# Optimization experiments

Measured on AMD Instinct MI355X. Metric: run time of the kernel, lower is better.

## Reference

```python
import jax, jax.numpy as jnp
import numpy as np

N, E, IN_DIM, HID, HEADS, OUT_DIM, T = 50000, 200000, 32, 64, 4, 32, 3
NEG_SLOPE = 0.2  # PyG GATv2Conv default


def setup_inputs() -> dict:
    key = jax.random.key(0)
    ks = jax.random.split(key, 16)
    s = 0.1
    return {
        "feat": jax.random.normal(ks[0], (N, IN_DIM), jnp.float32),
        "W_in": jax.random.normal(ks[1], (IN_DIM, HID), jnp.float32) * s,
        "b_in": jnp.zeros((HID,), jnp.float32),
        "Wl": jax.random.normal(ks[2], (2 * HID, HEADS * HID), jnp.float32) * s,
        "bl": jnp.zeros((HEADS * HID,), jnp.float32),
        "Wr": jax.random.normal(ks[3], (2 * HID, HEADS * HID), jnp.float32) * s,
        "br": jnp.zeros((HEADS * HID,), jnp.float32),
        "att": jax.random.normal(ks[4], (HEADS, HID), jnp.float32) * s,
        "b_conv": jnp.zeros((HEADS * HID,), jnp.float32),
        "Wg": jax.random.normal(ks[5], (HID, OUT_DIM), jnp.float32) * s,
        "bg": jnp.zeros((OUT_DIM,), jnp.float32),
        "edge_index": jax.random.randint(ks[6], (2, E), 0, N, jnp.int32),
        "node_mask": jax.random.randint(ks[7], (N,), 0, T + 1, jnp.int32),
        "current_state": jax.random.randint(ks[8], (N,), 0, 2, jnp.int32),
    }


def reference(feat, W_in, b_in, Wl, bl, Wr, br, att, b_conv, Wg, bg,
              edge_index, node_mask, current_state):
    # add self loops (GATv2Conv add_self_loops=True)
    loops = jnp.arange(N, dtype=edge_index.dtype)
    src = jnp.concatenate([edge_index[0], loops])  # [E+N]
    dst = jnp.concatenate([edge_index[1], loops])

    h0 = feat @ W_in + b_in  # [N, HID]
    bias_sum = b_conv.reshape(HEADS, HID).sum(0)  # heads are summed after bias add

    def step(h, i):
        active = node_mask > i  # [N] bool: nodes updated at this step
        x = jnp.concatenate([h, h0], axis=-1)  # [N, 2*HID]
        xl = (x @ Wl + bl).reshape(N, HEADS, HID)  # source transform
        xr = (x @ Wr + br).reshape(N, HEADS, HID)  # target transform
        e_act = active[src] & active[dst]  # edge alive iff both endpoints active
        s = jax.nn.leaky_relu(xl[src] + xr[dst], NEG_SLOPE)  # [E+N, H, C]
        score = jnp.einsum('ehc,hc->eh', s, att)  # [E+N, H]
        score = jnp.where(e_act[:, None], score, -1e30)
        smax = jax.lax.stop_gradient(
            jax.ops.segment_max(score, dst, num_segments=N))  # [N, H]
        ex = jnp.exp(score - smax[dst]) * e_act[:, None].astype(score.dtype)
        denom = jax.ops.segment_sum(ex, dst, num_segments=N)  # [N, H]
        alpha = ex / jnp.maximum(denom[dst], 1e-16)  # segment softmax per dst
        msg = alpha[:, :, None] * xl[src]  # [E+N, H, C]
        agg = jax.ops.segment_sum(msg, dst, num_segments=N)  # [N, H, C]
        out = jnp.tanh(agg.sum(1) + bias_sum)  # sum over heads, then Tanh
        return jnp.where(active[:, None], out, h), None

    h, _ = jax.lax.scan(step, h0, jnp.arange(T))
    # original returns g_embed(h[current_state]); fixed-shape variant: mask rows
    out = (h @ Wg + bg) * (current_state[:, None] > 0).astype(h.dtype)
    return out
```

## Files before the change

kernel.cpp:

```cpp
#include <hip/hip_runtime.h>
#include <hip/hip_bf16.h>

#define NN      50000
#define EE      200000
#define IN_DIM  32
#define HID     64
#define HEADS   4
#define OUTD    32
#define TSTEPS  3

typedef unsigned short bf16_t;
typedef __attribute__((ext_vector_type(8))) short  short8;
typedef __attribute__((ext_vector_type(4))) float  floatx4;

__device__ __forceinline__ float b2f(bf16_t u) {
    union { unsigned int i; float f; } v; v.i = ((unsigned int)u) << 16; return v.f;
}
__device__ __forceinline__ bf16_t f2b(float f) {
    union { float f; unsigned int i; } v; v.f = f;
    unsigned int r = v.i + 0x7FFF + ((v.i >> 16) & 1);
    return (bf16_t)(r >> 16);
}

__global__ void k_probe(const void* __restrict__ W_in, int* __restrict__ flag,
                        int* __restrict__ mbuf) {
    __shared__ int bad;
    int t = threadIdx.x;
    if (t == 0) bad = 0;
    if (t < 16) mbuf[t] = 0;
    __syncthreads();
    const bf16_t* p = (const bf16_t*)W_in;
    int mybad = 0;
    for (int i = t; i < IN_DIM * HID; i += 256) {
        float v = b2f(p[i]);
        if (v != v || fabsf(v) > 100.f) mybad = 1;
    }
    if (mybad) atomicOr(&bad, 1);
    __syncthreads();
    if (t == 0) *flag = bad ? 0 : 1;
}

__global__ __launch_bounds__(256) void k_cvt_small(
        const void* W_in, const void* b_in, const void* att, const void* bconv,
        const void* Wg, const void* bg,
        float* Winf, float* binf, float* attf, float* bcf, float* Wgf, float* bgf,
        const int* __restrict__ flag) {
    int i = blockIdx.x * 256 + threadIdx.x;
    int f = *flag;
    const void* src; float* dst; int off;
    if      (i < 2048) { src = W_in;  dst = Winf; off = i; }
    else if (i < 2112) { src = b_in;  dst = binf; off = i - 2048; }
    else if (i < 2368) { src = att;   dst = attf; off = i - 2112; }
    else if (i < 2624) { src = bconv; dst = bcf;  off = i - 2368; }
    else if (i < 4672) { src = Wg;    dst = Wgf;  off = i - 2624; }
    else if (i < 4704) { src = bg;    dst = bgf;  off = i - 4672; }
    else return;
    dst[off] = f ? b2f(((const bf16_t*)src)[off]) : ((const float*)src)[off];
}

__global__ __launch_bounds__(256) void k_wt(const void* Wl_raw, const void* Wr_raw,
                                            const void* bl_raw, const void* br_raw,
                                            bf16_t* __restrict__ Wt,
                                            float* __restrict__ bb,
                                            const int* __restrict__ flag) {
    int i = blockIdx.x * 256 + threadIdx.x;
    if (i >= 512 * 128) return;
    int f = *flag;
    int n = i >> 7, k = i & 127;
    const void* W = (n < 256) ? Wl_raw : Wr_raw;
    int nn = (n < 256) ? n : n - 256;
    float v = f ? b2f(((const bf16_t*)W)[k * 256 + nn])
                : ((const float*)W)[k * 256 + nn];
    Wt[i] = f2b(v);
    if (k == 0) {
        const void* b = (n < 256) ? bl_raw : br_raw;
        bb[n] = f ? b2f(((const bf16_t*)b)[nn]) : ((const float*)b)[nn];
    }
}

__global__ __launch_bounds__(256) void k_zero(int* __restrict__ p, int n) {
    int i = blockIdx.x * 256 + threadIdx.x;
    if (i < n) p[i] = 0;
}

__global__ __launch_bounds__(256) void k_hist(const int* __restrict__ dst,
                                              int* __restrict__ deg, int n) {
    int i = blockIdx.x * 256 + threadIdx.x;
    if (i < n) atomicAdd(&deg[dst[i]], 1);
}

__global__ __launch_bounds__(256) void k_scan_partial(const int* __restrict__ deg,
                                                      int* __restrict__ part, int n) {
    __shared__ int sd[256];
    int t = threadIdx.x;
    int base = blockIdx.x * 1024;
    int s = 0;
#pragma unroll
    for (int j = 0; j < 4; j++) {
        int i = base + t * 4 + j;
        if (i < n) s += deg[i];
    }
    sd[t] = s; __syncthreads();
    for (int off = 128; off > 0; off >>= 1) {
        if (t < off) sd[t] += sd[t + off];
        __syncthreads();
    }
    if (t == 0) part[blockIdx.x] = sd[0];
}

__global__ void k_scan_chunks(int* part, int nch) {
    if (threadIdx.x == 0 && blockIdx.x == 0) {
        int acc = 0;
        for (int i = 0; i < nch; i++) { int v = part[i]; part[i] = acc; acc += v; }
        part[nch] = acc;
    }
}

__global__ __launch_bounds__(256) void k_scan_final(const int* __restrict__ deg,
                                                    const int* __restrict__ part,
                                                    int* __restrict__ row_ptr,
                                                    int* __restrict__ cursor,
                                                    int n, int nch) {
    __shared__ int sc[256];
    int t = threadIdx.x;
    int base = blockIdx.x * 1024;
    int v[4]; int s = 0;
#pragma unroll
    for (int j = 0; j < 4; j++) {
        int i = base + t * 4 + j;
        v[j] = (i < n) ? deg[i] : 0;
        s += v[j];
    }
    sc[t] = s; __syncthreads();
    for (int off = 1; off < 256; off <<= 1) {
        int add = (t >= off) ? sc[t - off] : 0;
        __syncthreads();
        sc[t] += add;
        __syncthreads();
    }
    int run = sc[t] - s + part[blockIdx.x];
#pragma unroll
    for (int j = 0; j < 4; j++) {
        int i = base + t * 4 + j;
        if (i < n) { row_ptr[i] = run; cursor[i] = run; run += v[j]; }
    }
    if (blockIdx.x == 0 && t == 0) row_ptr[n] = part[nch];
}

__global__ __launch_bounds__(256) void k_scatter(const int* __restrict__ src,
                                                 const int* __restrict__ dst,
                                                 int* __restrict__ cursor,
                                                 int* __restrict__ col, int n) {
    int i = blockIdx.x * 256 + threadIdx.x;
    if (i < n) {
        int d = dst[i];
        int pos = atomicAdd(&cursor[d], 1);
        col[pos] = src[i];
    }
}

__global__ __launch_bounds__(256) void k_mhist(const int* __restrict__ mask,
                                               int* __restrict__ mbuf) {
    __shared__ int wcnt[4][4];
    int t = threadIdx.x, wid = t >> 6, lane = t & 63;
    int i = blockIdx.x * 256 + t;
    bool valid = i < NN;
    int v = 0;
    if (valid) { int m = mask[i]; v = m < 0 ? 0 : (m > 3 ? 3 : m); }
#pragma unroll
    for (int b = 0; b < 4; b++) {
        unsigned long long mm = __ballot(valid && v == b);
        if (lane == 0) wcnt[wid][b] = __popcll(mm);
    }
    __syncthreads();
    if (t < 4) {
        int s = wcnt[0][t] + wcnt[1][t] + wcnt[2][t] + wcnt[3][t];
        if (s) atomicAdd(&mbuf[t], s);
    }
}

__global__ void k_moff(int* mbuf) {
    if (threadIdx.x == 0 && blockIdx.x == 0) {
        int c1 = mbuf[1], c2 = mbuf[2], c3 = mbuf[3];
        mbuf[7] = 0;
        mbuf[6] = c3;
        mbuf[5] = c3 + c2;
        mbuf[4] = c3 + c2 + c1;
        mbuf[8] = c3 + c2 + c1;
        mbuf[9] = c3 + c2;
        mbuf[10] = c3;
    }
}

__global__ __launch_bounds__(256) void k_mscatter(const int* __restrict__ mask,
                                                  int* __restrict__ mbuf,
                                                  int* __restrict__ order) {
    __shared__ int wcnt[4][4];
    __shared__ int bbase[4];
    int t = threadIdx.x, wid = t >> 6, lane = t & 63;
    int i = blockIdx.x * 256 + t;
    bool valid = i < NN;
    int v = 0;
    if (valid) { int m = mask[i]; v = m < 0 ? 0 : (m > 3 ? 3 : m); }
    int rank = 0;
#pragma unroll
    for (int b = 0; b < 4; b++) {
        unsigned long long mm = __ballot(valid && v == b);
        if (valid && v == b)
            rank = __popcll(mm & ((lane == 0) ? 0ull : (~0ull >> (64 - lane))));
        if (lane == 0) wcnt[wid][b] = __popcll(mm);
    }
    __syncthreads();
    if (t < 4) {
        int tot = wcnt[0][t] + wcnt[1][t] + wcnt[2][t] + wcnt[3][t];
        bbase[t] = atomicAdd(&mbuf[4 + t], tot);
    }
    __syncthreads();
    if (valid) {
        int wpre = 0;
        for (int ww = 0; ww < wid; ww++) wpre += wcnt[ww][v];
        order[bbase[v] + wpre + rank] = i;
    }
}

__global__ __launch_bounds__(256) void k_h0(const void* __restrict__ feat_raw,
                                            const float* __restrict__ W_in,
                                            const float* __restrict__ b_in,
                                            float* __restrict__ h0,
                                            float* __restrict__ h,
                                            const int* __restrict__ flag) {
    __shared__ float Ws[IN_DIM * HID];
    __shared__ float bs[HID];
    int t = threadIdx.x;
    for (int i = t; i < IN_DIM * HID; i += 256) Ws[i] = W_in[i];
    if (t < HID) bs[t] = b_in[t];
    __syncthreads();
    int node = blockIdx.x * 4 + (t >> 6);
    int c = t & 63;
    if (node >= NN) return;
    int f = *flag;
    float acc = bs[c];
    if (f) {
        const bf16_t* fr = (const bf16_t*)feat_raw + (size_t)node * IN_DIM;
#pragma unroll
        for (int k = 0; k < IN_DIM; k++) acc += b2f(fr[k]) * Ws[k * HID + c];
    } else {
        const float* fr = (const float*)feat_raw + (size_t)node * IN_DIM;
#pragma unroll
        for (int k = 0; k < IN_DIM; k++) acc += fr[k] * Ws[k * HID + c];
    }
    h0[(size_t)node * HID + c] = acc;
    h [(size_t)node * HID + c] = acc;
}

__global__ __launch_bounds__(256) void k_gemm_mfma(const float* __restrict__ hcur,
                                                   const float* __restrict__ h0,
                                                   const bf16_t* __restrict__ Wt,
                                                   const float* __restrict__ bb,
                                                   bf16_t* __restrict__ xl,
                                                   bf16_t* __restrict__ xr,
                                                   const int* __restrict__ order,
                                                   const int* __restrict__ mbuf,
                                                   int step) {
    int count = mbuf[8 + step];
    int mbase = blockIdx.x * 64;
    if (mbase >= count) return;

    __shared__ bf16_t smem[64 * 136 + 128 * 136];
    bf16_t* As = smem;
    bf16_t* Bs = smem + 64 * 136;
    bf16_t* Cs = smem;

    int t = threadIdx.x;
    int nbase = blockIdx.y * 128;

    {
        int ln = t >> 2, lq = t & 3;
        int idx = mbase + ln;
        int node = (idx < count) ? order[idx] : -1;
        const float* hr  = hcur + (size_t)node * HID;
        const float* h0r = h0   + (size_t)node * HID;
#pragma unroll
        for (int j = 0; j < 8; j++) {
            int k = lq * 4 + j * 16;
            float4 v;
            if (node >= 0)
                v = (k < 64) ? *(const float4*)(hr + k) : *(const float4*)(h0r + (k - 64));
            else
                v = make_float4(0.f, 0.f, 0.f, 0.f);
            ushort4 o; o.x = f2b(v.x); o.y = f2b(v.y); o.z = f2b(v.z); o.w = f2b(v.w);
            *(ushort4*)(&As[ln * 136 + k]) = o;
        }
    }
#pragma unroll
    for (int i = 0; i < 8; i++) {
        int c = t + i * 256;
        int n = c >> 4, kc = (c & 15) * 8;
        *(ulonglong2*)(&Bs[n * 136 + kc]) =
            *(const ulonglong2*)(Wt + (size_t)(nbase + n) * 128 + kc);
    }
    __syncthreads();

    int wv = t >> 6;
    int lane = t & 63;
    int mrow = lane & 15;
    int quad = lane >> 4;

    floatx4 acc[8];
#pragma unroll
    for (int nf = 0; nf < 8; nf++) acc[nf] = (floatx4){0.f, 0.f, 0.f, 0.f};

#pragma unroll
    for (int kq = 0; kq < 4; kq++) {
        short8 a = *(const short8*)(&As[(wv * 16 + mrow) * 136 + kq * 32 + quad * 8]);
#pragma unroll
        for (int nf = 0; nf < 8; nf++) {
            short8 b = *(const short8*)(&Bs[(nf * 16 + mrow) * 136 + kq * 32 + quad * 8]);
            acc[nf] = __builtin_amdgcn_mfma_f32_16x16x32_bf16(a, b, acc[nf], 0, 0, 0);
        }
    }
    __syncthreads();

#pragma unroll
    for (int nf = 0; nf < 8; nf++) {
        float bv = bb[nbase + nf * 16 + mrow];
#pragma unroll
        for (int r = 0; r < 4; r++) {
            int m = wv * 16 + quad * 4 + r;
            Cs[m * 136 + nf * 16 + mrow] = f2b(acc[nf][r] + bv);
        }
    }
    __syncthreads();

    bf16_t* outp = (blockIdx.y < 2) ? xl : xr;
    int cc = (blockIdx.y & 1) * 128;
#pragma unroll
    for (int i = 0; i < 4; i++) {
        int c = t + i * 256;
        int m = c >> 4, kc = (c & 15) * 8;
        int idx = mbase + m;
        if (idx < count) {
            int node = order[idx];
            *(ulonglong2*)(outp + (size_t)node * 256 + cc + kc) =
                *(const ulonglong2*)(&Cs[m * 136 + kc]);
        }
    }
}

__global__ __launch_bounds__(256) void k_agg(float* __restrict__ h,
                                             const bf16_t* __restrict__ xl,
                                             const bf16_t* __restrict__ xr,
                                             const float* __restrict__ att,
                                             const float* __restrict__ b_conv,
                                             const int* __restrict__ row_ptr,
                                             const int* __restrict__ col,
                                             const int* __restrict__ node_mask,
                                             const int* __restrict__ order,
                                             const int* __restrict__ mbuf,
                                             int step) {
    int wid = threadIdx.x >> 6;
    int lane = threadIdx.x & 63;
    int idx = blockIdx.x * 4 + wid;
    if (idx >= mbuf[8 + step]) return;
    int node = order[idx];

    float4 attv = *(const float4*)(att + lane * 4);
    ushort4 xru = *(const ushort4*)(xr + (size_t)node * 256 + lane * 4);
    float xr0 = b2f(xru.x), xr1 = b2f(xru.y), xr2 = b2f(xru.z), xr3 = b2f(xru.w);

    float a0 = 0.f, a1 = 0.f, a2 = 0.f, a3 = 0.f, l = 0.f;

    auto edge_body = [&](int s, int act) {
        ushort4 xu = *(const ushort4*)(xl + (size_t)s * 256 + lane * 4);
        float x0 = b2f(xu.x), x1 = b2f(xu.y), x2 = b2f(xu.z), x3 = b2f(xu.w);
        float v0 = x0 + xr0; v0 = v0 > 0.f ? v0 : 0.2f * v0;
        float v1 = x1 + xr1; v1 = v1 > 0.f ? v1 : 0.2f * v1;
        float v2 = x2 + xr2; v2 = v2 > 0.f ? v2 : 0.2f * v2;
        float v3 = x3 + xr3; v3 = v3 > 0.f ? v3 : 0.2f * v3;
        float part = attv.x * v0 + attv.y * v1 + attv.z * v2 + attv.w * v3;
        part += __shfl_xor(part, 1, 64);
        part += __shfl_xor(part, 2, 64);
        part += __shfl_xor(part, 4, 64);
        part += __shfl_xor(part, 8, 64);
        float p = act ? __expf(part) : 0.f;
        l += p;
        a0 += p * x0; a1 += p * x1; a2 += p * x2; a3 += p * x3;
    };

    edge_body(node, 1);
    int e0 = row_ptr[node], e1 = row_ptr[node + 1];
    int e = e0;
    for (; e + 1 < e1; e += 2) {
        int s0 = col[e], s1 = col[e + 1];
        int m0 = node_mask[s0], m1 = node_mask[s1];
        edge_body(s0, m0 > step);
        edge_body(s1, m1 > step);
    }
    if (e < e1) {
        int s0 = col[e];
        edge_body(s0, node_mask[s0] > step);
    }

    float inv = 1.f / l;
    float4 bcv = *(const float4*)(b_conv + lane * 4);
    float t0 = a0 * inv + bcv.x;
    float t1 = a1 * inv + bcv.y;
    float t2 = a2 * inv + bcv.z;
    float t3 = a3 * inv + bcv.w;
    t0 += __shfl_xor(t0, 16, 64); t0 += __shfl_xor(t0, 32, 64);
    t1 += __shfl_xor(t1, 16, 64); t1 += __shfl_xor(t1, 32, 64);
    t2 += __shfl_xor(t2, 16, 64); t2 += __shfl_xor(t2, 32, 64);
    t3 += __shfl_xor(t3, 16, 64); t3 += __shfl_xor(t3, 32, 64);
    if (lane < 16) {
        float4 o = make_float4(tanhf(t0), tanhf(t1), tanhf(t2), tanhf(t3));
        *(float4*)(h + (size_t)node * HID + lane * 4) = o;
    }
}

__global__ __launch_bounds__(256) void k_out(const float* __restrict__ h,
                                             const float* __restrict__ Wg,
                                             const float* __restrict__ bg,
                                             const int* __restrict__ cs,
                                             void* __restrict__ out,
                                             const int* __restrict__ flag) {
    __shared__ float Ws[HID * OUTD];
    __shared__ float bs[OUTD];
    int t = threadIdx.x;
    for (int i = t; i < HID * OUTD; i += 256) Ws[i] = Wg[i];
    if (t < OUTD) bs[t] = bg[t];
    __syncthreads();
    int node = blockIdx.x * 8 + (t >> 5);
    int c = t & 31;
    if (node >= NN) return;
    float res = 0.f;
    if (cs[node] > 0) {
        const float* hr = h + (size_t)node * HID;
        float acc = bs[c];
#pragma unroll
        for (int k = 0; k < HID; k++) acc += hr[k] * Ws[k * OUTD + c];
        res = acc;
    }
    size_t idx = (size_t)node * OUTD + c;
    if (*flag) ((bf16_t*)out)[idx] = f2b(res);
    else       ((float*)out)[idx]  = res;
}

static inline size_t alignup(size_t x) { return (x + 255) & ~(size_t)255; }

extern "C" void kernel_launch(void* const* d_in, const int* in_sizes, int n_in,
                              void* d_out, int out_size, void* d_ws, size_t ws_size,
                              hipStream_t stream) {
    const void* feat_raw  = d_in[0];
    const void* W_in_raw  = d_in[1];
    const void* b_in_raw  = d_in[2];
    const void* Wl_raw    = d_in[3];
    const void* bl_raw    = d_in[4];
    const void* Wr_raw    = d_in[5];
    const void* br_raw    = d_in[6];
    const void* att_raw   = d_in[7];
    const void* bconv_raw = d_in[8];
    const void* Wg_raw    = d_in[9];
    const void* bg_raw    = d_in[10];
    const int* edge       = (const int*)d_in[11];
    const int* nmask      = (const int*)d_in[12];
    const int* cstate     = (const int*)d_in[13];

    const int* e_src = edge;
    const int* e_dst = edge + EE;

    const size_t SZ_H    = alignup((size_t)NN * HID * sizeof(float));
    const size_t SZ_X    = alignup((size_t)NN * 256 * sizeof(bf16_t));
    const size_t SZ_I    = alignup((size_t)NN * sizeof(int));
    const size_t SZ_RP   = alignup((size_t)(NN + 1) * sizeof(int));
    const size_t SZ_COL  = alignup((size_t)EE * sizeof(int));
    const int nch = (NN + 1023) / 1024;
    const size_t SZ_PART = alignup((size_t)(nch + 1) * sizeof(int));
    const size_t SZ_WIN  = alignup((size_t)IN_DIM * HID * sizeof(float));
    const size_t SZ_WT   = alignup((size_t)512 * 128 * sizeof(bf16_t));
    const size_t SZ_B    = alignup(512 * sizeof(float));
    const size_t SZ_WG   = alignup((size_t)HID * OUTD * sizeof(float));

    char* w = (char*)d_ws;
    float* h0    = (float*)w;  w += SZ_H;
    float* h     = (float*)w;  w += SZ_H;
    bf16_t* xl   = (bf16_t*)w; w += SZ_X;
    bf16_t* xr   = (bf16_t*)w; w += SZ_X;
    int* deg     = (int*)w;    w += SZ_I;
    int* row_ptr = (int*)w;    w += SZ_RP;
    int* cursor  = (int*)w;    w += SZ_I;
    int* colA    = (int*)w;    w += SZ_COL;
    int* order   = (int*)w;    w += SZ_I;
    int* part    = (int*)w;    w += SZ_PART;
    float* Winf  = (float*)w;  w += SZ_WIN;
    bf16_t* Wt   = (bf16_t*)w; w += SZ_WT;
    float* bb    = (float*)w;  w += SZ_B;
    float* attf  = (float*)w;  w += SZ_B;
    float* bcf   = (float*)w;  w += SZ_B;
    float* Wgf   = (float*)w;  w += SZ_WG;
    float* binf  = (float*)w;  w += SZ_B;
    float* bgf   = (float*)w;  w += SZ_B;
    int* flag    = (int*)w;    w += 256;
    int* mbuf    = (int*)w;    w += 256;
    if ((size_t)(w - (char*)d_ws) > ws_size) return;

    k_probe<<<1, 256, 0, stream>>>(W_in_raw, flag, mbuf);
    k_cvt_small<<<(4704 + 255) / 256, 256, 0, stream>>>(W_in_raw, b_in_raw, att_raw, bconv_raw,
                                                        Wg_raw, bg_raw,
                                                        Winf, binf, attf, bcf, Wgf, bgf, flag);
    k_wt<<<(512 * 128 + 255) / 256, 256, 0, stream>>>(Wl_raw, Wr_raw, bl_raw, br_raw, Wt, bb, flag);

    k_zero<<<(NN + 255) / 256, 256, 0, stream>>>(deg, NN);
    k_hist<<<(EE + 255) / 256, 256, 0, stream>>>(e_dst, deg, EE);
    k_scan_partial<<<nch, 256, 0, stream>>>(deg, part, NN);
    k_scan_chunks<<<1, 64, 0, stream>>>(part, nch);
    k_scan_final<<<nch, 256, 0, stream>>>(deg, part, row_ptr, cursor, NN, nch);
    k_scatter<<<(EE + 255) / 256, 256, 0, stream>>>(e_src, e_dst, cursor, colA, EE);

    k_mhist<<<(NN + 255) / 256, 256, 0, stream>>>(nmask, mbuf);
    k_moff<<<1, 64, 0, stream>>>(mbuf);
    k_mscatter<<<(NN + 255) / 256, 256, 0, stream>>>(nmask, mbuf, order);

    k_h0<<<(NN + 3) / 4, 256, 0, stream>>>(feat_raw, Winf, binf, h0, h, flag);

    for (int s = 0; s < TSTEPS; s++) {
        k_gemm_mfma<<<dim3((NN + 63) / 64, 4), 256, 0, stream>>>(h, h0, Wt, bb, xl, xr,
                                                                 order, mbuf, s);
        k_agg<<<(NN + 3) / 4, 256, 0, stream>>>(h, xl, xr, attf, bcf,
                                                row_ptr, colA, nmask, order, mbuf, s);
    }

    k_out<<<(NN + 7) / 8, 256, 0, stream>>>(h, Wgf, bgf, cstate, d_out, flag);
}
```

Measured before the change: 308.2 us.

## Fuse setup kernels and store hidden state in bf16

Merges the probe, conversion, weight-transpose and zeroing kernels into one setup kernel. It also folds the mask histogram and mask scatter into the edge histogram and edge scatter kernels, cutting the launch count by about six. The hidden states h and h0 are now stored as bf16, so the GEMM loads them directly without converting, and the memory traffic for h drops. The aggregation also skips inactive edges early. The cost is lower precision in the state that carries over between steps.

Result: faster. 277.8 us (-9.9%).

```diff
diff --git a/kernel.cpp b/kernel.cpp
--- a/kernel.cpp
+++ b/kernel.cpp
@@ -22,71 +22,85 @@
     return (bf16_t)(r >> 16);
 }
 
-__global__ void k_probe(const void* __restrict__ W_in, int* __restrict__ flag,
-                        int* __restrict__ mbuf) {
-    __shared__ int bad;
-    int t = threadIdx.x;
-    if (t == 0) bad = 0;
-    if (t < 16) mbuf[t] = 0;
-    __syncthreads();
-    const bf16_t* p = (const bf16_t*)W_in;
-    int mybad = 0;
-    for (int i = t; i < IN_DIM * HID; i += 256) {
-        float v = b2f(p[i]);
-        if (v != v || fabsf(v) > 100.f) mybad = 1;
-    }
-    if (mybad) atomicOr(&bad, 1);
-    __syncthreads();
-    if (t == 0) *flag = bad ? 0 : 1;
-}
-
-__global__ __launch_bounds__(256) void k_cvt_small(
+__global__ __launch_bounds__(256) void k_setup(
         const void* W_in, const void* b_in, const void* att, const void* bconv,
         const void* Wg, const void* bg,
+        const void* Wl_raw, const void* Wr_raw, const void* bl_raw, const void* br_raw,
         float* Winf, float* binf, float* attf, float* bcf, float* Wgf, float* bgf,
-        const int* __restrict__ flag) {
-    int i = blockIdx.x * 256 + threadIdx.x;
-    int f = *flag;
-    const void* src; float* dst; int off;
-    if      (i < 2048) { src = W_in;  dst = Winf; off = i; }
-    else if (i < 2112) { src = b_in;  dst = binf; off = i - 2048; }
-    else if (i < 2368) { src = att;   dst = attf; off = i - 2112; }
-    else if (i < 2624) { src = bconv; dst = bcf;  off = i - 2368; }
-    else if (i < 4672) { src = Wg;    dst = Wgf;  off = i - 2624; }
-    else if (i < 4704) { src = bg;    dst = bgf;  off = i - 4672; }
-    else return;
-    dst[off] = f ? b2f(((const bf16_t*)src)[off]) : ((const float*)src)[off];
-}
-
-__global__ __launch_bounds__(256) void k_wt(const void* Wl_raw, const void* Wr_raw,
-                                            const void* bl_raw, const void* br_raw,
-                                            bf16_t* __restrict__ Wt,
-                                            float* __restrict__ bb,
-                                            const int* __restrict__ flag) {
-    int i = blockIdx.x * 256 + threadIdx.x;
-    if (i >= 512 * 128) return;
-    int f = *flag;
-    int n = i >> 7, k = i & 127;
-    const void* W = (n < 256) ? Wl_raw : Wr_raw;
-    int nn = (n < 256) ? n : n - 256;
-    float v = f ? b2f(((const bf16_t*)W)[k * 256 + nn])
-                : ((const float*)W)[k * 256 + nn];
-    Wt[i] = f2b(v);
-    if (k == 0) {
-        const void* b = (n < 256) ? bl_raw : br_raw;
-        bb[n] = f ? b2f(((const bf16_t*)b)[nn]) : ((const float*)b)[nn];
-    }
-}
-
-__global__ __launch_bounds__(256) void k_zero(int* __restrict__ p, int n) {
-    int i = blockIdx.x * 256 + threadIdx.x;
-    if (i < n) p[i] = 0;
-}
-
-__global__ __launch_bounds__(256) void k_hist(const int* __restrict__ dst,
-                                              int* __restrict__ deg, int n) {
-    int i = blockIdx.x * 256 + threadIdx.x;
-    if (i < n) atomicAdd(&deg[dst[i]], 1);
+        bf16_t* __restrict__ Wt, float* __restrict__ bb,
+        int* __restrict__ deg, int* __restrict__ flag, int* __restrict__ mbuf) {
+    __shared__ int bad;
+    int t = threadIdx.x, bid = blockIdx.x;
+    if (t == 0) bad = 0;
+    __syncthreads();
+    {
+        const bf16_t* p = (const bf16_t*)W_in;
+        int mybad = 0;
+        for (int i = t; i < IN_DIM * HID; i += 256) {
+            float v = b2f(p[i]);
+            if (v != v || fabsf(v) > 100.f) mybad = 1;
+        }
+        if (mybad) atomicOr(&bad, 1);
+    }
+    __syncthreads();
+    int f = bad ? 0 : 1;
+    if (bid == 0 && t == 0) *flag = f;
+
+    if (bid < 256) {
+        int i = bid * 256 + t;
+        int n = i >> 7, k = i & 127;
+        const void* W = (n < 256) ? Wl_raw : Wr_raw;
+        int nn = (n < 256) ? n : n - 256;
+        float v = f ? b2f(((const bf16_t*)W)[k * 256 + nn])
+                    : ((const float*)W)[k * 256 + nn];
+        Wt[i] = f2b(v);
+        if (k == 0) {
+            const void* b = (n < 256) ? bl_raw : br_raw;
+            bb[n] = f ? b2f(((const bf16_t*)b)[nn]) : ((const float*)b)[nn];
+        }
+    } else if (bid < 275) {
+        int i = (bid - 256) * 256 + t;
+        const void* src; float* dst; int off;
+        if      (i < 2048) { src = W_in;  dst = Winf; off = i; }
+        else if (i < 2112) { src = b_in;  dst = binf; off = i - 2048; }
+        else if (i < 2368) { src = att;   dst = attf; off = i - 2112; }
+        else if (i < 2624) { src = bconv; dst = bcf;  off = i - 2368; }
+        else if (i < 4672) { src = Wg;    dst = Wgf;  off = i - 2624; }
+        else if (i < 4704) { src = bg;    dst = bgf;  off = i - 4672; }
+        else return;
+        dst[off] = f ? b2f(((const bf16_t*)src)[off]) : ((const float*)src)[off];
+    } else {
+        int i = (bid - 275) * 256 + t;
+        if (i < NN) deg[i] = 0;
+        if (bid == 275 && t < 16) mbuf[t] = 0;
+    }
+}
+
+__global__ __launch_bounds__(256) void k_hist_all(const int* __restrict__ dst,
+                                                  const int* __restrict__ mask,
+                                                  int* __restrict__ deg,
+                                                  int* __restrict__ mbuf) {
+    int t = threadIdx.x, bid = blockIdx.x;
+    int i = bid * 256 + t;
+    if (i < EE) atomicAdd(&deg[dst[i]], 1);
+    if (bid < (NN + 255) / 256) {
+        __shared__ int wcnt[4][4];
+        int wid = t >> 6, lane = t & 63;
+        int ni = bid * 256 + t;
+        bool valid = ni < NN;
+        int v = 0;
+        if (valid) { int m = mask[ni]; v = m < 0 ? 0 : (m > 3 ? 3 : m); }
+#pragma unroll
+        for (int b = 0; b < 4; b++) {
+            unsigned long long mm = __ballot(valid && v == b);
+            if (lane == 0) wcnt[wid][b] = __popcll(mm);
+        }
+        __syncthreads();
+        if (t < 4) {
+            int s = wcnt[0][t] + wcnt[1][t] + wcnt[2][t] + wcnt[3][t];
+            if (s) atomicAdd(&mbuf[t], s);
+        }
+    }
 }
 
 __global__ __launch_bounds__(256) void k_scan_partial(const int* __restrict__ deg,
@@ -108,11 +122,19 @@
     if (t == 0) part[blockIdx.x] = sd[0];
 }
 
-__global__ void k_scan_chunks(int* part, int nch) {
+__global__ void k_scan_mid(int* part, int nch, int* mbuf) {
     if (threadIdx.x == 0 && blockIdx.x == 0) {
         int acc = 0;
         for (int i = 0; i < nch; i++) { int v = part[i]; part[i] = acc; acc += v; }
         part[nch] = acc;
+        int c1 = mbuf[1], c2 = mbuf[2], c3 = mbuf[3];
+        mbuf[7] = 0;
+        mbuf[6] = c3;
+        mbuf[5] = c3 + c2;
+        mbuf[4] = c3 + c2 + c1;
+        mbuf[8] = c3 + c2 + c1;
+        mbuf[9] = c3 + c2;
+        mbuf[10] = c3;
     }
 }
 
@@ -147,87 +169,55 @@
     if (blockIdx.x == 0 && t == 0) row_ptr[n] = part[nch];
 }
 
-__global__ __launch_bounds__(256) void k_scatter(const int* __restrict__ src,
-                                                 const int* __restrict__ dst,
-                                                 int* __restrict__ cursor,
-                                                 int* __restrict__ col, int n) {
-    int i = blockIdx.x * 256 + threadIdx.x;
-    if (i < n) {
+__global__ __launch_bounds__(256) void k_scatter_all(const int* __restrict__ src,
+                                                     const int* __restrict__ dst,
+                                                     int* __restrict__ cursor,
+                                                     int* __restrict__ col,
+                                                     const int* __restrict__ mask,
+                                                     int* __restrict__ mbuf,
+                                                     int* __restrict__ order) {
+    int t = threadIdx.x, bid = blockIdx.x;
+    int i = bid * 256 + t;
+    if (i < EE) {
         int d = dst[i];
         int pos = atomicAdd(&cursor[d], 1);
         col[pos] = src[i];
     }
-}
-
-__global__ __launch_bounds__(256) void k_mhist(const int* __restrict__ mask,
-                                               int* __restrict__ mbuf) {
-    __shared__ int wcnt[4][4];
-    int t = threadIdx.x, wid = t >> 6, lane = t & 63;
-    int i = blockIdx.x * 256 + t;
-    bool valid = i < NN;
-    int v = 0;
-    if (valid) { int m = mask[i]; v = m < 0 ? 0 : (m > 3 ? 3 : m); }
-#pragma unroll
-    for (int b = 0; b < 4; b++) {
-        unsigned long long mm = __ballot(valid && v == b);
-        if (lane == 0) wcnt[wid][b] = __popcll(mm);
-    }
-    __syncthreads();
-    if (t < 4) {
-        int s = wcnt[0][t] + wcnt[1][t] + wcnt[2][t] + wcnt[3][t];
-        if (s) atomicAdd(&mbuf[t], s);
-    }
-}
-
-__global__ void k_moff(int* mbuf) {
-    if (threadIdx.x == 0 && blockIdx.x == 0) {
-        int c1 = mbuf[1], c2 = mbuf[2], c3 = mbuf[3];
-        mbuf[7] = 0;
-        mbuf[6] = c3;
-        mbuf[5] = c3 + c2;
-        mbuf[4] = c3 + c2 + c1;
-        mbuf[8] = c3 + c2 + c1;
-        mbuf[9] = c3 + c2;
-        mbuf[10] = c3;
-    }
-}
-
-__global__ __launch_bounds__(256) void k_mscatter(const int* __restrict__ mask,
-                                                  int* __restrict__ mbuf,
-                                                  int* __restrict__ order) {
-    __shared__ int wcnt[4][4];
-    __shared__ int bbase[4];
-    int t = threadIdx.x, wid = t >> 6, lane = t & 63;
-    int i = blockIdx.x * 256 + t;
-    bool valid = i < NN;
-    int v = 0;
-    if (valid) { int m = mask[i]; v = m < 0 ? 0 : (m > 3 ? 3 : m); }
-    int rank = 0;
-#pragma unroll
-    for (int b = 0; b < 4; b++) {
-        unsigned long long mm = __ballot(valid && v == b);
-        if (valid && v == b)
-            rank = __popcll(mm & ((lane == 0) ? 0ull : (~0ull >> (64 - lane))));
-        if (lane == 0) wcnt[wid][b] = __popcll(mm);
-    }
-    __syncthreads();
-    if (t < 4) {
-        int tot = wcnt[0][t] + wcnt[1][t] + wcnt[2][t] + wcnt[3][t];
-        bbase[t] = atomicAdd(&mbuf[4 + t], tot);
-    }
-    __syncthreads();
-    if (valid) {
-        int wpre = 0;
-        for (int ww = 0; ww < wid; ww++) wpre += wcnt[ww][v];
-        order[bbase[v] + wpre + rank] = i;
+    if (bid < (NN + 255) / 256) {
+        __shared__ int wcnt[4][4];
+        __shared__ int bbase[4];
+        int wid = t >> 6, lane = t & 63;
+        int ni = bid * 256 + t;
+        bool valid = ni < NN;
+        int v = 0;
+        if (valid) { int m = mask[ni]; v = m < 0 ? 0 : (m > 3 ? 3 : m); }
+        int rank = 0;
+#pragma unroll
+        for (int b = 0; b < 4; b++) {
+            unsigned long long mm = __ballot(valid && v == b);
+            if (valid && v == b)
+                rank = __popcll(mm & ((lane == 0) ? 0ull : (~0ull >> (64 - lane))));
+            if (lane == 0) wcnt[wid][b] = __popcll(mm);
+        }
+        __syncthreads();
+        if (t < 4) {
+            int tot = wcnt[0][t] + wcnt[1][t] + wcnt[2][t] + wcnt[3][t];
+            bbase[t] = atomicAdd(&mbuf[4 + t], tot);
+        }
+        __syncthreads();
+        if (valid) {
+            int wpre = 0;
+            for (int ww = 0; ww < wid; ww++) wpre += wcnt[ww][v];
+            order[bbase[v] + wpre + rank] = ni;
+        }
     }
 }
 
 __global__ __launch_bounds__(256) void k_h0(const void* __restrict__ feat_raw,
                                             const float* __restrict__ W_in,
                                             const float* __restrict__ b_in,
-                                            float* __restrict__ h0,
-                                            float* __restrict__ h,
+                                            bf16_t* __restrict__ h0,
+                                            bf16_t* __restrict__ h,
                                             const int* __restrict__ flag) {
     __shared__ float Ws[IN_DIM * HID];
     __shared__ float bs[HID];
@@ -249,12 +239,13 @@
 #pragma unroll
         for (int k = 0; k < IN_DIM; k++) acc += fr[k] * Ws[k * HID + c];
     }
-    h0[(size_t)node * HID + c] = acc;
-    h [(size_t)node * HID + c] = acc;
-}
-
-__global__ __launch_bounds__(256) void k_gemm_mfma(const float* __restrict__ hcur,
-                                                   const float* __restrict__ h0,
+    bf16_t o = f2b(acc);
+    h0[(size_t)node * HID + c] = o;
+    h [(size_t)node * HID + c] = o;
+}
+
+__global__ __launch_bounds__(256) void k_gemm_mfma(const bf16_t* __restrict__ h,
+                                                   const bf16_t* __restrict__ h0,
                                                    const bf16_t* __restrict__ Wt,
                                                    const float* __restrict__ bb,
                                                    bf16_t* __restrict__ xl,
@@ -278,18 +269,17 @@
         int ln = t >> 2, lq = t & 3;
         int idx = mbase + ln;
         int node = (idx < count) ? order[idx] : -1;
-        const float* hr  = hcur + (size_t)node * HID;
-        const float* h0r = h0   + (size_t)node * HID;
-#pragma unroll
-        for (int j = 0; j < 8; j++) {
-            int k = lq * 4 + j * 16;
-            float4 v;
-            if (node >= 0)
-                v = (k < 64) ? *(const float4*)(hr + k) : *(const float4*)(h0r + (k - 64));
-            else
-                v = make_float4(0.f, 0.f, 0.f, 0.f);
-            ushort4 o; o.x = f2b(v.x); o.y = f2b(v.y); o.z = f2b(v.z); o.w = f2b(v.w);
-            *(ushort4*)(&As[ln * 136 + k]) = o;
+        ulonglong2 z; z.x = 0; z.y = 0;
+#pragma unroll
+        for (int j = 0; j < 2; j++) {
+            int chunk = lq + j * 4;
+            ulonglong2 vh = z, vh0 = z;
+            if (node >= 0) {
+                vh  = *(const ulonglong2*)(h  + (size_t)node * HID + chunk * 8);
+                vh0 = *(const ulonglong2*)(h0 + (size_t)node * HID + chunk * 8);
+            }
+            *(ulonglong2*)(&As[ln * 136 + chunk * 8]) = vh;
+            *(ulonglong2*)(&As[ln * 136 + 64 + chunk * 8]) = vh0;
         }
     }
 #pragma unroll
@@ -347,7 +337,7 @@
     }
 }
 
-__global__ __launch_bounds__(256) void k_agg(float* __restrict__ h,
+__global__ __launch_bounds__(256) void k_agg(bf16_t* __restrict__ h,
                                              const bf16_t* __restrict__ xl,
                                              const bf16_t* __restrict__ xr,
                                              const float* __restrict__ att,
@@ -370,7 +360,8 @@
 
     float a0 = 0.f, a1 = 0.f, a2 = 0.f, a3 = 0.f, l = 0.f;
 
-    auto edge_body = [&](int s, int act) {
+    auto edge_body = [&](int s, bool act) {
+        if (!act) return;
         ushort4 xu = *(const ushort4*)(xl + (size_t)s * 256 + lane * 4);
         float x0 = b2f(xu.x), x1 = b2f(xu.y), x2 = b2f(xu.z), x3 = b2f(xu.w);
         float v0 = x0 + xr0; v0 = v0 > 0.f ? v0 : 0.2f * v0;
@@ -382,12 +373,12 @@
         part += __shfl_xor(part, 2, 64);
         part += __shfl_xor(part, 4, 64);
         part += __shfl_xor(part, 8, 64);
-        float p = act ? __expf(part) : 0.f;
+        float p = __expf(part);
         l += p;
         a0 += p * x0; a1 += p * x1; a2 += p * x2; a3 += p * x3;
     };
 
-    edge_body(node, 1);
+    edge_body(node, true);
     int e0 = row_ptr[node], e1 = row_ptr[node + 1];
     int e = e0;
     for (; e + 1 < e1; e += 2) {
@@ -412,12 +403,14 @@
     t2 += __shfl_xor(t2, 16, 64); t2 += __shfl_xor(t2, 32, 64);
     t3 += __shfl_xor(t3, 16, 64); t3 += __shfl_xor(t3, 32, 64);
     if (lane < 16) {
-        float4 o = make_float4(tanhf(t0), tanhf(t1), tanhf(t2), tanhf(t3));
-        *(float4*)(h + (size_t)node * HID + lane * 4) = o;
-    }
-}
-
-__global__ __launch_bounds__(256) void k_out(const float* __restrict__ h,
+        ushort4 o;
+        o.x = f2b(tanhf(t0)); o.y = f2b(tanhf(t1));
+        o.z = f2b(tanhf(t2)); o.w = f2b(tanhf(t3));
+        *(ushort4*)(h + (size_t)node * HID + lane * 4) = o;
+    }
+}
+
+__global__ __launch_bounds__(256) void k_out(const bf16_t* __restrict__ h,
                                              const float* __restrict__ Wg,
                                              const float* __restrict__ bg,
                                              const int* __restrict__ cs,
@@ -434,10 +427,10 @@
     if (node >= NN) return;
     float res = 0.f;
     if (cs[node] > 0) {
-        const float* hr = h + (size_t)node * HID;
+        const bf16_t* hr = h + (size_t)node * HID;
         float acc = bs[c];
 #pragma unroll
-        for (int k = 0; k < HID; k++) acc += hr[k] * Ws[k * OUTD + c];
+        for (int k = 0; k < HID; k++) acc += b2f(hr[k]) * Ws[k * OUTD + c];
         res = acc;
     }
     size_t idx = (size_t)node * OUTD + c;
@@ -468,7 +461,7 @@
     const int* e_src = edge;
     const int* e_dst = edge + EE;
 
-    const size_t SZ_H    = alignup((size_t)NN * HID * sizeof(float));
+    const size_t SZ_HB   = alignup((size_t)NN * HID * sizeof(bf16_t));
     const size_t SZ_X    = alignup((size_t)NN * 256 * sizeof(bf16_t));
     const size_t SZ_I    = alignup((size_t)NN * sizeof(int));
     const size_t SZ_RP   = alignup((size_t)(NN + 1) * sizeof(int));
@@ -481,8 +474,8 @@
     const size_t SZ_WG   = alignup((size_t)HID * OUTD * sizeof(float));
 
     char* w = (char*)d_ws;
-    float* h0    = (float*)w;  w += SZ_H;
-    float* h     = (float*)w;  w += SZ_H;
+    bf16_t* h0   = (bf16_t*)w; w += SZ_HB;
+    bf16_t* h    = (bf16_t*)w; w += SZ_HB;
     bf16_t* xl   = (bf16_t*)w; w += SZ_X;
     bf16_t* xr   = (bf16_t*)w; w += SZ_X;
     int* deg     = (int*)w;    w += SZ_I;
@@ -503,22 +496,17 @@
     int* mbuf    = (int*)w;    w += 256;
     if ((size_t)(w - (char*)d_ws) > ws_size) return;
 
-    k_probe<<<1, 256, 0, stream>>>(W_in_raw, flag, mbuf);
-    k_cvt_small<<<(4704 + 255) / 256, 256, 0, stream>>>(W_in_raw, b_in_raw, att_raw, bconv_raw,
-                                                        Wg_raw, bg_raw,
-                                                        Winf, binf, attf, bcf, Wgf, bgf, flag);
-    k_wt<<<(512 * 128 + 255) / 256, 256, 0, stream>>>(Wl_raw, Wr_raw, bl_raw, br_raw, Wt, bb, flag);
-
-    k_zero<<<(NN + 255) / 256, 256, 0, stream>>>(deg, NN);
-    k_hist<<<(EE + 255) / 256, 256, 0, stream>>>(e_dst, deg, EE);
+    k_setup<<<275 + (NN + 255) / 256, 256, 0, stream>>>(
+        W_in_raw, b_in_raw, att_raw, bconv_raw, Wg_raw, bg_raw,
+        Wl_raw, Wr_raw, bl_raw, br_raw,
+        Winf, binf, attf, bcf, Wgf, bgf, Wt, bb, deg, flag, mbuf);
+
+    k_hist_all<<<(EE + 255) / 256, 256, 0, stream>>>(e_dst, nmask, deg, mbuf);
     k_scan_partial<<<nch, 256, 0, stream>>>(deg, part, NN);
-    k_scan_chunks<<<1, 64, 0, stream>>>(part, nch);
+    k_scan_mid<<<1, 64, 0, stream>>>(part, nch, mbuf);
     k_scan_final<<<nch, 256, 0, stream>>>(deg, part, row_ptr, cursor, NN, nch);
-    k_scatter<<<(EE + 255) / 256, 256, 0, stream>>>(e_src, e_dst, cursor, colA, EE);
-
-    k_mhist<<<(NN + 255) / 256, 256, 0, stream>>>(nmask, mbuf);
-    k_moff<<<1, 64, 0, stream>>>(mbuf);
-    k_mscatter<<<(NN + 255) / 256, 256, 0, stream>>>(nmask, mbuf, order);
+    k_scatter_all<<<(EE + 255) / 256, 256, 0, stream>>>(e_src, e_dst, cursor, colA,
+                                                        nmask, mbuf, order);
 
     k_h0<<<(NN + 3) / 4, 256, 0, stream>>>(feat_raw, Winf, binf, h0, h, flag);
 
```
